# Kernel optimization log

Measured on AMD Instinct MI355X. Metric: run time of the kernel, lower is better.

The kernel has to match this reference:

```python
import jax, jax.numpy as jnp
import numpy as np

N_DENSE = 13
N_SPARSE = 26
FIELD_FEAT = 10000
FIELD_NUM = N_DENSE + N_SPARSE  # 39
FEATURE_NUM = N_DENSE + N_SPARSE * FIELD_FEAT  # 260013
K = 16
BATCH = 4096


def setup_inputs() -> dict:
    key = jax.random.key(0)
    k1, k2, k3, k4 = jax.random.split(key, 4)
    dense = jax.random.uniform(k1, (BATCH, N_DENSE), dtype=jnp.float32)
    sparse = jax.random.randint(k2, (BATCH, N_SPARSE), 0, FIELD_FEAT).astype(jnp.float32)
    x = jnp.concatenate([dense, sparse], axis=1)  # [B, field_num]
    # xavier-ish scale for embeddings
    W = jax.random.normal(k3, (FIELD_NUM, FEATURE_NUM, K), dtype=jnp.float32) * 0.01
    fc_w = jax.random.normal(k4, (FEATURE_NUM, 1), dtype=jnp.float32) * 0.01
    bias = jnp.zeros((1,), dtype=jnp.float32)
    field_features = np.array([1] * N_DENSE + [FIELD_FEAT] * N_SPARSE)
    offsets = jnp.asarray(np.concatenate([[0], np.cumsum(field_features)[:-1]]), dtype=jnp.int32)
    return {"x": x, "W": W, "fc_w": fc_w, "bias": bias, "offsets": offsets, "n_dense": N_DENSE}


def reference(x, W, fc_w, bias, offsets, n_dense):
    B, F = x.shape
    # build global feature indices: dense columns -> index 0 (+offset), sparse keep value
    idx = jnp.floor(x).astype(jnp.int32)
    idx = idx.at[:, :n_dense].set(0)
    x_f = idx + offsets[None, :]  # [B, F]
    # field-aware gather: E[i, b, j] = W[i][x_f[b, j]]  -> [F, B, F, K]
    E = jnp.take(W, x_f, axis=1)
    # pairwise dots: dot[b, i, j] = <E[i, b, j], E[j, b, i]>
    dot = jnp.einsum('ibjk,jbik->bij', E, E)  # [B, F, F]
    # multiplier: dense value for dense fields, 1 for sparse fields
    x_m = jnp.concatenate([x[:, :n_dense], jnp.ones((B, F - n_dense), dtype=x.dtype)], axis=1)
    w_pair = x_m[:, :, None] * x_m[:, None, :]  # [B, F, F]
    # original loops: i in [0, F-2], j in [0, F-1] (full j range, faithfully kept)
    row_mask = (jnp.arange(F) < F - 1).astype(x.dtype)[None, :, None]  # [1, F, 1]
    cross = jnp.sum(dot * w_pair * row_mask, axis=(1, 2), keepdims=False)[:, None]  # [B, 1]
    linear = jnp.sum(fc_w[x_f], axis=1) + bias  # [B, 1]
    return jax.nn.sigmoid(linear + cross)
```

## Files before the change

### kernel.cpp

```cpp
#include <hip/hip_runtime.h>
#include <math.h>

#define NF 39
#define ND 13
#define KDIM 16
#define FEAT 260013
#define NPAIRS (NF * (NF + 1) / 2)

__global__ __launch_bounds__(256) void ffm_kernel(
    const float* __restrict__ x,
    const float* __restrict__ W,
    const float* __restrict__ fc_w,
    const float* __restrict__ bias,
    const int*   __restrict__ offsets,
    float* __restrict__ out,
    int B)
{
    __shared__ int   sf[NF];
    __shared__ float sxm[NF];
    __shared__ unsigned char spi[NPAIRS];
    __shared__ unsigned char spj[NPAIRS];
    __shared__ float sred[4];

    const int b   = blockIdx.x;
    const int tid = threadIdx.x;

    if (tid < NF) {
        float xv = x[(size_t)b * NF + tid];
        int idx  = (tid < ND) ? 0 : (int)floorf(xv);
        sf[tid]  = idx + offsets[tid];
        sxm[tid] = (tid < ND) ? xv : 1.0f;
    }
    for (int p = tid; p < NPAIRS; p += blockDim.x) {
        int i = 0, base = 0;
        while (p >= base + (NF - i)) { base += NF - i; ++i; }
        spi[p] = (unsigned char)i;
        spj[p] = (unsigned char)(i + (p - base));
    }
    __syncthreads();

    float acc = 0.0f;

    if (tid < NF) acc += fc_w[sf[tid]];

    for (int p = tid; p < NPAIRS; p += blockDim.x) {
        const int i = spi[p];
        const int j = spj[p];
        if (i == NF - 1) continue;

        float w;
        if (i == j)            w = sxm[i] * sxm[i];
        else if (j < NF - 1)   w = 2.0f * sxm[i] * sxm[j];
        else                   w = sxm[i] * sxm[j];

        const float4* vij = (const float4*)(W + ((size_t)i * FEAT + sf[j]) * KDIM);
        const float4* vji = (const float4*)(W + ((size_t)j * FEAT + sf[i]) * KDIM);

        float d = 0.0f;
        #pragma unroll
        for (int q = 0; q < 4; ++q) {
            float4 a = vij[q];
            float4 c = vji[q];
            d += a.x * c.x + a.y * c.y + a.z * c.z + a.w * c.w;
        }
        acc += w * d;
    }

    #pragma unroll
    for (int off = 32; off > 0; off >>= 1)
        acc += __shfl_down(acc, off, 64);
    if ((tid & 63) == 0) sred[tid >> 6] = acc;
    __syncthreads();

    if (tid == 0) {
        float z = sred[0] + sred[1] + sred[2] + sred[3] + bias[0];
        out[b] = 1.0f / (1.0f + expf(-z));
    }
}

extern "C" void kernel_launch(void* const* d_in, const int* in_sizes, int n_in,
                              void* d_out, int out_size, void* d_ws, size_t ws_size,
                              hipStream_t stream) {
    const float* x       = (const float*)d_in[0];
    const float* W       = (const float*)d_in[1];
    const float* fc_w    = (const float*)d_in[2];
    const float* bias    = (const float*)d_in[3];
    const int*   offsets = (const int*)d_in[4];

    float* out = (float*)d_out;
    const int B = in_sizes[0] / NF;

    ffm_kernel<<<B, 256, 0, stream>>>(x, W, fc_w, bias, offsets, out, B);
}
```

Before: 791.6 us.

## Spread each pair's embedding loads across eight lanes with shuffle-based dot product

Each pair is now handled by 8 threads: two groups of four lanes each load one float4 of the two 64-byte embedding vectors. The dot product is formed by exchanging values with xor shuffles, and the pair loop is unrolled over fixed passes with padding pairs given zero weight. The aim is coalesced 64-byte accesses and more loads in flight, replacing eight scattered float4 loads per thread. In exchange each pair term is computed twice and halved, and each pass adds shuffle instructions.

Measured after the change: 784.4 us. Within noise of the previous version (-0.9%).

```diff
diff --git a/kernel.cpp b/kernel.cpp
--- a/kernel.cpp
+++ b/kernel.cpp
@@ -6,6 +6,7 @@
 #define KDIM 16
 #define FEAT 260013
 #define NPAIRS (NF * (NF + 1) / 2)
+#define PASSES ((NPAIRS + 31) / 32)
 
 __global__ __launch_bounds__(256) void ffm_kernel(
     const float* __restrict__ x,
@@ -16,11 +17,10 @@
     float* __restrict__ out,
     int B)
 {
-    __shared__ int   sf[NF];
-    __shared__ float sxm[NF];
-    __shared__ unsigned char spi[NPAIRS];
-    __shared__ unsigned char spj[NPAIRS];
-    __shared__ float sred[4];
+    __shared__ int            sf[NF];
+    __shared__ float          sxm[NF];
+    __shared__ unsigned short spij[NPAIRS];
+    __shared__ float          sred[4];
 
     const int b   = blockIdx.x;
     const int tid = threadIdx.x;
@@ -31,39 +31,48 @@
         sf[tid]  = idx + offsets[tid];
         sxm[tid] = (tid < ND) ? xv : 1.0f;
     }
-    for (int p = tid; p < NPAIRS; p += blockDim.x) {
+    for (int p = tid; p < NPAIRS; p += 256) {
         int i = 0, base = 0;
         while (p >= base + (NF - i)) { base += NF - i; ++i; }
-        spi[p] = (unsigned char)i;
-        spj[p] = (unsigned char)(i + (p - base));
+        int j = i + (p - base);
+        spij[p] = (unsigned short)(i | (j << 8));
     }
     __syncthreads();
 
+    const int slot = tid >> 3;
+    const int quad = (tid >> 2) & 1;
+    const int qi   = tid & 3;
+
     float acc = 0.0f;
-
     if (tid < NF) acc += fc_w[sf[tid]];
 
-    for (int p = tid; p < NPAIRS; p += blockDim.x) {
-        const int i = spi[p];
-        const int j = spj[p];
-        if (i == NF - 1) continue;
+    #pragma unroll 5
+    for (int pass = 0; pass < PASSES; ++pass) {
+        int p  = pass * 32 + slot;
+        int pc = (p < NPAIRS) ? p : (NPAIRS - 1);
+        int ij = spij[pc];
+        int i  = ij & 0xff;
+        int j  = ij >> 8;
 
         float w;
-        if (i == j)            w = sxm[i] * sxm[i];
+        if (i == j)            w = (i < NF - 1) ? sxm[i] * sxm[i] : 0.0f;
         else if (j < NF - 1)   w = 2.0f * sxm[i] * sxm[j];
         else                   w = sxm[i] * sxm[j];
+        if (p >= NPAIRS) w = 0.0f;
 
-        const float4* vij = (const float4*)(W + ((size_t)i * FEAT + sf[j]) * KDIM);
-        const float4* vji = (const float4*)(W + ((size_t)j * FEAT + sf[i]) * KDIM);
+        int row  = quad ? j : i;
+        int feat = quad ? sf[i] : sf[j];
+        const float4* vp = (const float4*)(W + ((size_t)row * FEAT + feat) * KDIM);
+        float4 v = vp[qi];
 
-        float d = 0.0f;
-        #pragma unroll
-        for (int q = 0; q < 4; ++q) {
-            float4 a = vij[q];
-            float4 c = vji[q];
-            d += a.x * c.x + a.y * c.y + a.z * c.z + a.w * c.w;
-        }
-        acc += w * d;
+        float4 u;
+        u.x = __shfl_xor(v.x, 4, 64);
+        u.y = __shfl_xor(v.y, 4, 64);
+        u.z = __shfl_xor(v.z, 4, 64);
+        u.w = __shfl_xor(v.w, 4, 64);
+
+        float d = v.x * u.x + v.y * u.y + v.z * u.z + v.w * u.w;
+        acc += 0.5f * w * d;
     }
 
     #pragma unroll
```

## Split each pair's dot product across four lanes for coalesced embedding gathers

Applied to the files above, without the earlier changes.

Each embedding pair's 16-float dot product is now split across four adjacent threads, each loading one float4, so a quad reads a contiguous 64-byte row. Pair offsets and weights are precomputed into shared memory, and the pair loop is fully unrolled into fixed passes. The aim is better coalescing and more outstanding loads for the random gathers. In exchange it uses more shared memory and redundant index work, and padded tail slots do clamped loads.

Result: no change. 787.6 us (-0.5%).

```diff
diff --git a/kernel.cpp b/kernel.cpp
--- a/kernel.cpp
+++ b/kernel.cpp
@@ -6,6 +6,8 @@
 #define KDIM 16
 #define FEAT 260013
 #define NPAIRS (NF * (NF + 1) / 2)
+#define PAIRS_PER_PASS 64
+#define PASSES ((NPAIRS + PAIRS_PER_PASS - 1) / PAIRS_PER_PASS)
 
 __global__ __launch_bounds__(256) void ffm_kernel(
     const float* __restrict__ x,
@@ -18,8 +20,9 @@
 {
     __shared__ int   sf[NF];
     __shared__ float sxm[NF];
-    __shared__ unsigned char spi[NPAIRS];
-    __shared__ unsigned char spj[NPAIRS];
+    __shared__ int   soff_ij[NPAIRS];
+    __shared__ int   soff_ji[NPAIRS];
+    __shared__ float sw[NPAIRS];
     __shared__ float sred[4];
 
     const int b   = blockIdx.x;
@@ -31,39 +34,40 @@
         sf[tid]  = idx + offsets[tid];
         sxm[tid] = (tid < ND) ? xv : 1.0f;
     }
-    for (int p = tid; p < NPAIRS; p += blockDim.x) {
+    __syncthreads();
+
+    for (int p = tid; p < NPAIRS; p += 256) {
         int i = 0, base = 0;
         while (p >= base + (NF - i)) { base += NF - i; ++i; }
-        spi[p] = (unsigned char)i;
-        spj[p] = (unsigned char)(i + (p - base));
+        int j = i + (p - base);
+        soff_ij[p] = (i * FEAT + sf[j]) * KDIM;
+        soff_ji[p] = (j * FEAT + sf[i]) * KDIM;
+        float w;
+        if (i == j)          w = (i < NF - 1) ? sxm[i] * sxm[i] : 0.0f;
+        else if (j < NF - 1) w = 2.0f * sxm[i] * sxm[j];
+        else                 w = sxm[i] * sxm[j];
+        sw[p] = w;
     }
     __syncthreads();
 
+    const int slot = tid >> 2;
+    const int qi   = tid & 3;
+
     float acc = 0.0f;
-
     if (tid < NF) acc += fc_w[sf[tid]];
 
-    for (int p = tid; p < NPAIRS; p += blockDim.x) {
-        const int i = spi[p];
-        const int j = spj[p];
-        if (i == NF - 1) continue;
+    #pragma unroll
+    for (int pass = 0; pass < PASSES; ++pass) {
+        int p  = pass * PAIRS_PER_PASS + slot;
+        int pc = (p < NPAIRS) ? p : (NPAIRS - 1);
+        float w = (p < NPAIRS) ? sw[pc] : 0.0f;
 
-        float w;
-        if (i == j)            w = sxm[i] * sxm[i];
-        else if (j < NF - 1)   w = 2.0f * sxm[i] * sxm[j];
-        else                   w = sxm[i] * sxm[j];
+        const float4* aij = (const float4*)(W + soff_ij[pc]);
+        const float4* cji = (const float4*)(W + soff_ji[pc]);
+        float4 a = aij[qi];
+        float4 c = cji[qi];
 
-        const float4* vij = (const float4*)(W + ((size_t)i * FEAT + sf[j]) * KDIM);
-        const float4* vji = (const float4*)(W + ((size_t)j * FEAT + sf[i]) * KDIM);
-
-        float d = 0.0f;
-        #pragma unroll
-        for (int q = 0; q < 4; ++q) {
-            float4 a = vij[q];
-            float4 c = vji[q];
-            d += a.x * c.x + a.y * c.y + a.z * c.z + a.w * c.w;
-        }
-        acc += w * d;
+        acc += w * (a.x * c.x + a.y * c.y + a.z * c.z + a.w * c.w);
     }
 
     #pragma unroll
```
